# Kernel optimization log

Hardware: AMD Instinct MI355X
Metric: run time of the kernel (lower is better)

Reference implementation:

```python
import jax, jax.numpy as jnp
import numpy as np

N, S1, S2, H, D = 2, 4096, 4096, 8, 64

def setup_inputs() -> dict:
    key = jax.random.key(0)
    kq, kk, kv = jax.random.split(key, 3)
    queries = jax.random.normal(kq, (N, S1, H, D), dtype=jnp.float32)
    keys = jax.random.normal(kk, (N, S2, H, D), dtype=jnp.float32)
    values = jax.random.normal(kv, (N, S2, H, D), dtype=jnp.float32)
    q_mask = jnp.ones((N, S1), dtype=bool)
    kv_mask = jnp.ones((N, S2), dtype=bool)
    return {"queries": queries, "keys": keys, "values": values,
            "q_mask": q_mask, "kv_mask": kv_mask}

def reference(queries, keys, values, q_mask, kv_mask):
    # queries: [N,L,H,D], keys/values: [N,S,H,D], masks: [N,L]/[N,S]
    scale = 1.0 / jnp.sqrt(jnp.asarray(queries.shape[3], queries.dtype))
    q = queries * scale
    qk = jnp.einsum('nlhd,nshd->nlsh', q, keys)  # [N,L,S,H]
    valid = q_mask[:, :, None, None] & kv_mask[:, None, :, None]  # [N,L,S,1]
    qk = jnp.where(valid, qk, -jnp.inf)
    attn = jax.nn.softmax(qk, axis=2)  # softmax over S
    out = jnp.einsum('nlsh,nshd->nlhd', attn, values)  # [N,L,H,D]
    return out
```

## Files before the change

### kernel.cpp

```cpp
#include <hip/hip_runtime.h>
#include <hip/hip_bf16.h>
#include <stdint.h>

#define NB 2
#define S1d 4096
#define S2d 4096
#define NH 8
#define DH 64

typedef float f32x4 __attribute__((ext_vector_type(4)));
typedef float f32x16 __attribute__((ext_vector_type(16)));
typedef __bf16 bf16x8 __attribute__((ext_vector_type(8)));
typedef __bf16 bf16x2 __attribute__((ext_vector_type(2)));
typedef unsigned short u16x8 __attribute__((ext_vector_type(8)));

__device__ __forceinline__ unsigned short f2bf(float f) {
    union { float f; uint32_t u; } v; v.f = f;
    uint32_t u = v.u;
    return (unsigned short)((u + 0x7fffu + ((u >> 16) & 1u)) >> 16);
}

__device__ __forceinline__ __bf16 to_bf(float x) { return (__bf16)x; }

__device__ __forceinline__ float E2(float x) {
#if __has_builtin(__builtin_amdgcn_exp2f)
    return __builtin_amdgcn_exp2f(x);
#else
    return __expf(x * 0.69314718055994531f);
#endif
}

#define GLDS(gp, lp) __builtin_amdgcn_global_load_lds( \
    (const __attribute__((address_space(1))) uint32_t*)(gp), \
    (__attribute__((address_space(3))) uint32_t*)(lp), 16, 0, 0)

#define SWAP32(a, b) asm volatile("v_permlane32_swap_b32 %0, %1" : "+v"(a), "+v"(b))

__global__ void prep_k(const float* __restrict__ k, unsigned short* __restrict__ kb) {
    int t = blockIdx.x * 256 + threadIdx.x;
    int dg = t & 15;
    int h  = (t >> 4) & 7;
    int s  = (t >> 7) & (S2d - 1);
    int n  = t >> 19;
    float4 v = *reinterpret_cast<const float4*>(k + ((((size_t)n * S2d + s) * NH + h) * DH) + dg * 4);
    ushort4 o;
    o.x = f2bf(v.x); o.y = f2bf(v.y); o.z = f2bf(v.z); o.w = f2bf(v.w);
    *reinterpret_cast<ushort4*>(kb + ((((size_t)n * NH + h) * S2d + s) * DH) + dg * 4) = o;
}

__global__ void prep_v(const float* __restrict__ v, unsigned short* __restrict__ vtb) {
    __shared__ unsigned short T[64][72];
    int st = blockIdx.x & 63;
    int h  = (blockIdx.x >> 6) & 7;
    int n  = blockIdx.x >> 9;
    int t  = threadIdx.x;
    {
        int r = t >> 2, dg = t & 3;
        const float* src = v + ((((size_t)n * S2d + st * 64 + r) * NH + h) * DH) + dg * 16;
#pragma unroll
        for (int i = 0; i < 4; i++) {
            float4 x = *reinterpret_cast<const float4*>(src + i * 4);
            int d = dg * 16 + i * 4;
            T[d + 0][r] = f2bf(x.x);
            T[d + 1][r] = f2bf(x.y);
            T[d + 2][r] = f2bf(x.z);
            T[d + 3][r] = f2bf(x.w);
        }
    }
    __syncthreads();
    {
        int d = t >> 2, sg = t & 3;
        const u16x8* rp = reinterpret_cast<const u16x8*>(&T[d][sg * 16]);
        u16x8 a = rp[0], b = rp[1];
        u16x8* wp = reinterpret_cast<u16x8*>(
            vtb + (((size_t)n * NH + h) * DH + d) * S2d + st * 64 + sg * 16);
        wp[0] = a; wp[1] = b;
    }
}

#define QSCALE 0.1803368801111204f

union WU { uint32_t u; bf16x2 v; };
union FR { uint32_t u[4]; bf16x8 v; };

#define PACKPAIR(SS, B, OUT) do {                                        \
    WU a_, b_, c_, d_;                                                   \
    a_.v[0] = to_bf(SS[B+0]); a_.v[1] = to_bf(SS[B+1]);                  \
    c_.v[0] = to_bf(SS[B+4]); c_.v[1] = to_bf(SS[B+5]);                  \
    SWAP32(a_.u, c_.u);                                                  \
    b_.v[0] = to_bf(SS[B+2]); b_.v[1] = to_bf(SS[B+3]);                  \
    d_.v[0] = to_bf(SS[B+6]); d_.v[1] = to_bf(SS[B+7]);                  \
    SWAP32(b_.u, d_.u);                                                  \
    OUT.u[0] = a_.u; OUT.u[1] = b_.u; OUT.u[2] = c_.u; OUT.u[3] = d_.u;  \
  } while (0)

__global__ __launch_bounds__(256, 4) void flash(
    const float* __restrict__ q, const unsigned short* __restrict__ kb,
    const unsigned short* __restrict__ vtb, float* __restrict__ out,
    float* __restrict__ pO1, float* __restrict__ sums) {

    __shared__ __align__(16) unsigned char smem[34816];

    int bid = blockIdx.x;
    int nh = (bid & 7) * 2 + ((bid >> 3) & 1);
    int qt = (bid >> 4) & 31;
    int kvhalf = bid >> 9;
    int n = nh >> 3, h = nh & 7;

    int tid = threadIdx.x;
    int lane = tid & 63, wid = tid >> 6;
    int l31 = lane & 31, h2 = lane >> 5, swz = lane & 7;

    const unsigned short* kbase = kb  + (size_t)nh * S2d * DH + (size_t)kvhalf * 2048 * DH;
    const unsigned short* vbase = vtb + (size_t)nh * DH * S2d + kvhalf * 2048;

    int g0 = wid * 128 + lane;
    int g1 = g0 + 64;
    int r0 = g0 >> 3, c0 = (g0 & 7) ^ (r0 & 7);
    int r1 = g1 >> 3, c1 = (g1 & 7) ^ (r1 & 7);
    const unsigned short* kg0 = kbase + r0 * DH + c0 * 8;
    const unsigned short* kg1 = kbase + r1 * DH + c1 * 8;
    const unsigned short* vg0 = vbase + (size_t)r0 * S2d + c0 * 8;
    const unsigned short* vg1 = vbase + (size_t)r1 * S2d + c1 * 8;

    {
        unsigned short* kl = (unsigned short*)smem;
        unsigned short* vl = (unsigned short*)(smem + 8192);
        GLDS(kg0, kl + (wid * 2 + 0) * 512);
        GLDS(kg1, kl + (wid * 2 + 1) * 512);
        GLDS(vg0, vl + (wid * 2 + 0) * 512);
        GLDS(vg1, vl + (wid * 2 + 1) * 512);
        kg0 += 64 * DH; kg1 += 64 * DH; vg0 += 64; vg1 += 64;
    }

    bf16x8 qf[4];
    {
        int qrow = qt * 128 + wid * 32 + l31;
        const float* qp = q + (((size_t)n * S1d + qrow) * NH + h) * DH;
#pragma unroll
        for (int kt = 0; kt < 4; kt++) {
            f32x4 x0 = *(const f32x4*)(qp + kt * 16 + h2 * 8);
            f32x4 x1 = *(const f32x4*)(qp + kt * 16 + h2 * 8 + 4);
            bf16x8 f;
#pragma unroll
            for (int j = 0; j < 4; j++) f[j] = to_bf(x0[j] * QSCALE);
#pragma unroll
            for (int j = 0; j < 4; j++) f[4 + j] = to_bf(x1[j] * QSCALE);
            qf[kt] = f;
        }
    }

    f32x16 o0, o1;
#pragma unroll
    for (int i = 0; i < 16; i++) { o0[i] = 0.f; o1[i] = 0.f; }
    float lsum = 0.f;

    __syncthreads();

    int cur = 0;
    for (int t = 0; t < 32; ++t) {
        if (t < 31) {
            unsigned short* kl = (unsigned short*)(smem + (cur ^ 1) * 16384);
            unsigned short* vl = (unsigned short*)(smem + (cur ^ 1) * 16384 + 8192);
            GLDS(kg0, kl + (wid * 2 + 0) * 512);
            GLDS(kg1, kl + (wid * 2 + 1) * 512);
            GLDS(vg0, vl + (wid * 2 + 0) * 512);
            GLDS(vg1, vl + (wid * 2 + 1) * 512);
            kg0 += 64 * DH; kg1 += 64 * DH; vg0 += 64; vg1 += 64;
        }

        const unsigned short* Kl = (const unsigned short*)(smem + cur * 16384);
        const unsigned short* Vl = (const unsigned short*)(smem + cur * 16384 + 8192);
        int pb = l31 * 64;

        f32x16 s0, s1;
        __builtin_amdgcn_s_setprio(1);
        {
            int gg = (h2 ^ swz) * 8;
            bf16x8 k0 = *(const bf16x8*)&Kl[pb + gg];
            bf16x8 k1 = *(const bf16x8*)&Kl[pb + 2048 + gg];
            f32x16 z;
#pragma unroll
            for (int i = 0; i < 16; i++) z[i] = 0.f;
            s0 = __builtin_amdgcn_mfma_f32_32x32x16_bf16(k0, qf[0], z, 0, 0, 0);
            s1 = __builtin_amdgcn_mfma_f32_32x32x16_bf16(k1, qf[0], z, 0, 0, 0);
        }
#pragma unroll
        for (int kt = 1; kt < 4; kt++) {
            int gg = ((kt * 2 + h2) ^ swz) * 8;
            bf16x8 k0 = *(const bf16x8*)&Kl[pb + gg];
            bf16x8 k1 = *(const bf16x8*)&Kl[pb + 2048 + gg];
            s0 = __builtin_amdgcn_mfma_f32_32x32x16_bf16(k0, qf[kt], s0, 0, 0, 0);
            s1 = __builtin_amdgcn_mfma_f32_32x32x16_bf16(k1, qf[kt], s1, 0, 0, 0);
        }
        __builtin_amdgcn_s_setprio(0);

#pragma unroll
        for (int i = 0; i < 16; i++) { s0[i] = E2(s0[i]); s1[i] = E2(s1[i]); }

        {
            float ta[16];
#pragma unroll
            for (int i = 0; i < 16; i++) ta[i] = s0[i] + s1[i];
#pragma unroll
            for (int st = 8; st > 0; st >>= 1)
#pragma unroll
                for (int i = 0; i < 8; i++) if (i < st) ta[i] += ta[i + st];
            lsum += ta[0];
        }

        FR pf0, pf1, pf2, pf3;
        PACKPAIR(s0, 0, pf0);
        PACKPAIR(s0, 8, pf1);
        PACKPAIR(s1, 0, pf2);
        PACKPAIR(s1, 8, pf3);

        __builtin_amdgcn_s_setprio(1);
#pragma unroll
        for (int kt = 0; kt < 4; kt++) {
            int gg = ((kt * 2 + h2) ^ swz) * 8;
            bf16x8 v0 = *(const bf16x8*)&Vl[pb + gg];
            bf16x8 v1 = *(const bf16x8*)&Vl[pb + 2048 + gg];
            bf16x8 pw = (kt == 0) ? pf0.v : (kt == 1) ? pf1.v : (kt == 2) ? pf2.v : pf3.v;
            o0 = __builtin_amdgcn_mfma_f32_32x32x16_bf16(v0, pw, o0, 0, 0, 0);
            o1 = __builtin_amdgcn_mfma_f32_32x32x16_bf16(v1, pw, o1, 0, 0, 0);
        }
        __builtin_amdgcn_s_setprio(0);

        __syncthreads();
        cur ^= 1;
    }

    float tot = lsum + __shfl_xor(lsum, 32);
    {
        int qrow = qt * 128 + wid * 32 + l31;
        if (h2 == 0)
            sums[(size_t)kvhalf * (NB * NH * S1d) + (size_t)nh * S1d + qrow] = tot;
    }

    float* OW = (float*)smem + wid * (32 * 68);
#pragma unroll
    for (int r = 0; r < 16; r++) {
        int d0 = (r & 3) + 8 * (r >> 2) + 4 * h2;
        OW[l31 * 68 + d0]      = o0[r];
        OW[l31 * 68 + 32 + d0] = o1[r];
    }
    __syncthreads();

    float* pO = kvhalf ? pO1 : out;
    int qrb = qt * 128 + wid * 32;
#pragma unroll
    for (int it = 0; it < 8; it++) {
        int idx = it * 64 + lane;
        int qq = idx >> 4, dg = idx & 15;
        f32x4 val = *(const f32x4*)&OW[qq * 68 + dg * 4];
        *(f32x4*)&pO[(((size_t)n * S1d + qrb + qq) * NH + h) * DH + dg * 4] = val;
    }
}

__global__ void combine(float* __restrict__ out, const float* __restrict__ pO1,
                        const float* __restrict__ sums) {
    int idx = blockIdx.x * 256 + threadIdx.x;
    int h = (idx >> 4) & 7, qv = (idx >> 7) & 4095, n = idx >> 19;
    size_t off = (size_t)idx * 4;
    f32x4 a = *(const f32x4*)(out + off);
    f32x4 b = *(const f32x4*)(pO1 + off);
    int nh = n * 8 + h;
    float s = sums[(size_t)nh * S1d + qv] + sums[(size_t)NB * NH * S1d + (size_t)nh * S1d + qv];
    float inv = 1.0f / s;
    f32x4 r;
    r[0] = (a[0] + b[0]) * inv;
    r[1] = (a[1] + b[1]) * inv;
    r[2] = (a[2] + b[2]) * inv;
    r[3] = (a[3] + b[3]) * inv;
    *(f32x4*)(out + off) = r;
}

extern "C" void kernel_launch(void* const* d_in, const int* in_sizes, int n_in,
                              void* d_out, int out_size, void* d_ws, size_t ws_size,
                              hipStream_t stream) {
    const float* q = (const float*)d_in[0];
    const float* k = (const float*)d_in[1];
    const float* v = (const float*)d_in[2];
    float* out = (float*)d_out;

    unsigned short* kb  = (unsigned short*)d_ws;
    unsigned short* vtb = kb + (size_t)NB * NH * S2d * DH;
    float* pO1  = (float*)(vtb + (size_t)NB * NH * S2d * DH);
    float* sums = pO1 + (size_t)NB * S1d * NH * DH;

    prep_k<<<4096, 256, 0, stream>>>(k, kb);
    prep_v<<<1024, 256, 0, stream>>>(v, vtb);
    flash<<<1024, 256, 0, stream>>>(q, kb, vtb, out, pO1, sums);
    combine<<<4096, 256, 0, stream>>>(out, pO1, sums);
}
```

Baseline: 101.9 us.

## Triple-buffer K/V tiles in LDS with explicit vmcnt waits and a single barrier

Replaces the double-buffered K/V staging loop with a three-buffer ring that keeps two tiles in flight. Each tile waits only on its own loads via an explicit s_waitcnt vmcnt and a single raw s_barrier, instead of a full __syncthreads after every tile. The aim is to hide global-to-LDS load latency more deeply and remove per-iteration synchronisation overhead. In exchange, LDS per block grows from 34816 to 49152 bytes, which may cap how many blocks fit on a CU under launch_bounds(256,4), and the loop is fully unrolled through macros.

```diff
diff --git a/kernel.cpp b/kernel.cpp
--- a/kernel.cpp
+++ b/kernel.cpp
@@ -94,12 +94,78 @@
     OUT.u[0] = a_.u; OUT.u[1] = b_.u; OUT.u[2] = c_.u; OUT.u[3] = d_.u;  \
   } while (0)
 
+#define STAGE(BUF) do {                                                  \
+    unsigned short* kl = (unsigned short*)(smem + (BUF) * 16384);        \
+    unsigned short* vl = (unsigned short*)(smem + (BUF) * 16384 + 8192); \
+    GLDS(kg0, kl + (wid * 2 + 0) * 512);                                 \
+    GLDS(kg1, kl + (wid * 2 + 1) * 512);                                 \
+    GLDS(vg0, vl + (wid * 2 + 0) * 512);                                 \
+    GLDS(vg1, vl + (wid * 2 + 1) * 512);                                 \
+    kg0 += 64 * DH; kg1 += 64 * DH; vg0 += 64; vg1 += 64;                \
+  } while (0)
+
+#define TILE(CURB, STGB, DOSTG, WNSTR) do {                                    \
+    asm volatile("s_waitcnt vmcnt(" WNSTR ")" ::: "memory");                   \
+    __builtin_amdgcn_s_barrier();                                              \
+    __builtin_amdgcn_sched_barrier(0);                                         \
+    if (DOSTG) STAGE(STGB);                                                    \
+    const unsigned short* Kl = (const unsigned short*)(smem + (CURB) * 16384); \
+    const unsigned short* Vl = (const unsigned short*)(smem + (CURB) * 16384 + 8192); \
+    int pb = l31 * 64;                                                         \
+    f32x16 s0, s1;                                                             \
+    __builtin_amdgcn_s_setprio(1);                                             \
+    {                                                                          \
+        int gg = (h2 ^ swz) * 8;                                               \
+        bf16x8 k0 = *(const bf16x8*)&Kl[pb + gg];                              \
+        bf16x8 k1 = *(const bf16x8*)&Kl[pb + 2048 + gg];                       \
+        s0 = __builtin_amdgcn_mfma_f32_32x32x16_bf16(k0, qf[0], zc, 0, 0, 0);  \
+        s1 = __builtin_amdgcn_mfma_f32_32x32x16_bf16(k1, qf[0], zc, 0, 0, 0);  \
+    }                                                                          \
+    _Pragma("unroll")                                                          \
+    for (int kt = 1; kt < 4; kt++) {                                           \
+        int gg = ((kt * 2 + h2) ^ swz) * 8;                                    \
+        bf16x8 k0 = *(const bf16x8*)&Kl[pb + gg];                              \
+        bf16x8 k1 = *(const bf16x8*)&Kl[pb + 2048 + gg];                       \
+        s0 = __builtin_amdgcn_mfma_f32_32x32x16_bf16(k0, qf[kt], s0, 0, 0, 0); \
+        s1 = __builtin_amdgcn_mfma_f32_32x32x16_bf16(k1, qf[kt], s1, 0, 0, 0); \
+    }                                                                          \
+    __builtin_amdgcn_s_setprio(0);                                             \
+    _Pragma("unroll")                                                          \
+    for (int i = 0; i < 16; i++) { s0[i] = E2(s0[i]); s1[i] = E2(s1[i]); }     \
+    {                                                                          \
+        float ta[16];                                                          \
+        _Pragma("unroll")                                                      \
+        for (int i = 0; i < 16; i++) ta[i] = s0[i] + s1[i];                    \
+        _Pragma("unroll")                                                      \
+        for (int st = 8; st > 0; st >>= 1)                                     \
+            _Pragma("unroll")                                                  \
+            for (int i = 0; i < 8; i++) if (i < st) ta[i] += ta[i + st];       \
+        lsum += ta[0];                                                         \
+    }                                                                          \
+    FR pf0, pf1, pf2, pf3;                                                     \
+    PACKPAIR(s0, 0, pf0);                                                      \
+    PACKPAIR(s0, 8, pf1);                                                      \
+    PACKPAIR(s1, 0, pf2);                                                      \
+    PACKPAIR(s1, 8, pf3);                                                      \
+    __builtin_amdgcn_s_setprio(1);                                             \
+    _Pragma("unroll")                                                          \
+    for (int kt = 0; kt < 4; kt++) {                                           \
+        int gg = ((kt * 2 + h2) ^ swz) * 8;                                    \
+        bf16x8 v0 = *(const bf16x8*)&Vl[pb + gg];                              \
+        bf16x8 v1 = *(const bf16x8*)&Vl[pb + 2048 + gg];                       \
+        bf16x8 pw = (kt == 0) ? pf0.v : (kt == 1) ? pf1.v : (kt == 2) ? pf2.v : pf3.v; \
+        o0 = __builtin_amdgcn_mfma_f32_32x32x16_bf16(v0, pw, o0, 0, 0, 0);     \
+        o1 = __builtin_amdgcn_mfma_f32_32x32x16_bf16(v1, pw, o1, 0, 0, 0);     \
+    }                                                                          \
+    __builtin_amdgcn_s_setprio(0);                                             \
+  } while (0)
+
 __global__ __launch_bounds__(256, 4) void flash(
     const float* __restrict__ q, const unsigned short* __restrict__ kb,
     const unsigned short* __restrict__ vtb, float* __restrict__ out,
     float* __restrict__ pO1, float* __restrict__ sums) {
 
-    __shared__ __align__(16) unsigned char smem[34816];
+    __shared__ __align__(16) unsigned char smem[49152];
 
     int bid = blockIdx.x;
     int nh = (bid & 7) * 2 + ((bid >> 3) & 1);
@@ -123,16 +189,6 @@
     const unsigned short* vg0 = vbase + (size_t)r0 * S2d + c0 * 8;
     const unsigned short* vg1 = vbase + (size_t)r1 * S2d + c1 * 8;
 
-    {
-        unsigned short* kl = (unsigned short*)smem;
-        unsigned short* vl = (unsigned short*)(smem + 8192);
-        GLDS(kg0, kl + (wid * 2 + 0) * 512);
-        GLDS(kg1, kl + (wid * 2 + 1) * 512);
-        GLDS(vg0, vl + (wid * 2 + 0) * 512);
-        GLDS(vg1, vl + (wid * 2 + 1) * 512);
-        kg0 += 64 * DH; kg1 += 64 * DH; vg0 += 64; vg1 += 64;
-    }
-
     bf16x8 qf[4];
     {
         int qrow = qt * 128 + wid * 32 + l31;
@@ -150,86 +206,24 @@
         }
     }
 
-    f32x16 o0, o1;
-#pragma unroll
-    for (int i = 0; i < 16; i++) { o0[i] = 0.f; o1[i] = 0.f; }
+    STAGE(0);
+    STAGE(1);
+
+    f32x16 zc;
+#pragma unroll
+    for (int i = 0; i < 16; i++) zc[i] = 0.f;
+    f32x16 o0 = zc, o1 = zc;
     float lsum = 0.f;
 
+    for (int it = 0; it < 10; ++it) {
+        TILE(0, 2, 1, "4");
+        TILE(1, 0, 1, "4");
+        TILE(2, 1, 1, "4");
+    }
+    TILE(0, 0, 0, "4");
+    TILE(1, 0, 0, "0");
+
     __syncthreads();
-
-    int cur = 0;
-    for (int t = 0; t < 32; ++t) {
-        if (t < 31) {
-            unsigned short* kl = (unsigned short*)(smem + (cur ^ 1) * 16384);
-            unsigned short* vl = (unsigned short*)(smem + (cur ^ 1) * 16384 + 8192);
-            GLDS(kg0, kl + (wid * 2 + 0) * 512);
-            GLDS(kg1, kl + (wid * 2 + 1) * 512);
-            GLDS(vg0, vl + (wid * 2 + 0) * 512);
-            GLDS(vg1, vl + (wid * 2 + 1) * 512);
-            kg0 += 64 * DH; kg1 += 64 * DH; vg0 += 64; vg1 += 64;
-        }
-
-        const unsigned short* Kl = (const unsigned short*)(smem + cur * 16384);
-        const unsigned short* Vl = (const unsigned short*)(smem + cur * 16384 + 8192);
-        int pb = l31 * 64;
-
-        f32x16 s0, s1;
-        __builtin_amdgcn_s_setprio(1);
-        {
-            int gg = (h2 ^ swz) * 8;
-            bf16x8 k0 = *(const bf16x8*)&Kl[pb + gg];
-            bf16x8 k1 = *(const bf16x8*)&Kl[pb + 2048 + gg];
-            f32x16 z;
-#pragma unroll
-            for (int i = 0; i < 16; i++) z[i] = 0.f;
-            s0 = __builtin_amdgcn_mfma_f32_32x32x16_bf16(k0, qf[0], z, 0, 0, 0);
-            s1 = __builtin_amdgcn_mfma_f32_32x32x16_bf16(k1, qf[0], z, 0, 0, 0);
-        }
-#pragma unroll
-        for (int kt = 1; kt < 4; kt++) {
-            int gg = ((kt * 2 + h2) ^ swz) * 8;
-            bf16x8 k0 = *(const bf16x8*)&Kl[pb + gg];
-            bf16x8 k1 = *(const bf16x8*)&Kl[pb + 2048 + gg];
-            s0 = __builtin_amdgcn_mfma_f32_32x32x16_bf16(k0, qf[kt], s0, 0, 0, 0);
-            s1 = __builtin_amdgcn_mfma_f32_32x32x16_bf16(k1, qf[kt], s1, 0, 0, 0);
-        }
-        __builtin_amdgcn_s_setprio(0);
-
-#pragma unroll
-        for (int i = 0; i < 16; i++) { s0[i] = E2(s0[i]); s1[i] = E2(s1[i]); }
-
-        {
-            float ta[16];
-#pragma unroll
-            for (int i = 0; i < 16; i++) ta[i] = s0[i] + s1[i];
-#pragma unroll
-            for (int st = 8; st > 0; st >>= 1)
-#pragma unroll
-                for (int i = 0; i < 8; i++) if (i < st) ta[i] += ta[i + st];
-            lsum += ta[0];
-        }
-
-        FR pf0, pf1, pf2, pf3;
-        PACKPAIR(s0, 0, pf0);
-        PACKPAIR(s0, 8, pf1);
-        PACKPAIR(s1, 0, pf2);
-        PACKPAIR(s1, 8, pf3);
-
-        __builtin_amdgcn_s_setprio(1);
-#pragma unroll
-        for (int kt = 0; kt < 4; kt++) {
-            int gg = ((kt * 2 + h2) ^ swz) * 8;
-            bf16x8 v0 = *(const bf16x8*)&Vl[pb + gg];
-            bf16x8 v1 = *(const bf16x8*)&Vl[pb + 2048 + gg];
-            bf16x8 pw = (kt == 0) ? pf0.v : (kt == 1) ? pf1.v : (kt == 2) ? pf2.v : pf3.v;
-            o0 = __builtin_amdgcn_mfma_f32_32x32x16_bf16(v0, pw, o0, 0, 0, 0);
-            o1 = __builtin_amdgcn_mfma_f32_32x32x16_bf16(v1, pw, o1, 0, 0, 0);
-        }
-        __builtin_amdgcn_s_setprio(0);
-
-        __syncthreads();
-        cur ^= 1;
-    }
 
     float tot = lsum + __shfl_xor(lsum, 32);
     {
```

After: 110.4 us. +8.3%, slower.
